# Optimization experiments

Measured on AMD Instinct MI355X. Metric: run time of the kernel, lower is better.

The kernel has to match this reference:

```python
import jax, jax.numpy as jnp
import numpy as np

N_Q, N_T, D, C = 4096, 8192, 512, 16
SIGMA = 2.0


def setup_inputs() -> dict:
    key = jax.random.key(0)
    k1, k2, k3 = jax.random.split(key, 3)
    X = jax.random.normal(k1, (N_Q, D), dtype=jnp.float32)
    X_train = jax.random.normal(k2, (N_T, D), dtype=jnp.float32)
    y = jax.random.randint(k3, (N_T,), 0, C, dtype=jnp.int32)
    sigma = jnp.float32(SIGMA)
    return {"X": X, "X_train": X_train, "y": y, "sigma": sigma}


def reference(X, X_train, y, sigma):
    xx = jnp.sum(X * X, axis=1, keepdims=True)              # [N_q, 1]
    tt = jnp.sum(X_train * X_train, axis=1)                 # [N_t]
    cross = jnp.einsum('qd,td->qt', X, X_train)             # [N_q, N_t]
    dist2 = jnp.maximum(xx + tt[None, :] - 2.0 * cross, 0.0)
    pattern = jnp.exp(-dist2 / (2.0 * sigma ** 2))          # Gaussian RBF kernel [N_q, N_t]
    # per-class segment sum over training patterns (replaces per-class Python loop)
    summation = jax.ops.segment_sum(pattern.T, y, num_segments=C).T  # [N_q, C]
    summation = summation / jnp.sum(summation, axis=1, keepdims=True)
    return jnp.argmax(summation, axis=1)
```

## Files before the change

### kernel.cpp

```cpp
#include <hip/hip_runtime.h>


#define NQ 4096
#define NT 8192
#define DD 512
#define NC 16
#define LN_FLT_MIN -87.336544750402f
#define SCREEN_T 730.0f

typedef __attribute__((ext_vector_type(4))) int   v4i;
typedef __attribute__((ext_vector_type(8))) int   v8i;
typedef __attribute__((ext_vector_type(16))) float f32x16;

__global__ __launch_bounds__(256) void prep_k(const float* __restrict__ X,
                                              const float* __restrict__ XT,
                                              unsigned char* __restrict__ fXp,
                                              unsigned char* __restrict__ fTp,
                                              float* __restrict__ xx,
                                              float* __restrict__ tt,
                                              float* __restrict__ classacc) {
  const int lane = threadIdx.x & 63;
  const int row  = blockIdx.x * 4 + (threadIdx.x >> 6);
  const float* src; unsigned char* dst; float* nrm; int r;
  if (row < NT) { r = row; src = XT + (size_t)r * DD; dst = fTp; nrm = tt + r; }
  else { r = row - NT; src = X + (size_t)r * DD; dst = fXp; nrm = xx + r; }
  const float4* s4 = (const float4*)src;
  const float4 a = s4[lane * 2], b = s4[lane * 2 + 1];
  int w0 = __builtin_amdgcn_cvt_pk_fp8_f32(a.x, a.y, 0, false);
  w0     = __builtin_amdgcn_cvt_pk_fp8_f32(a.z, a.w, w0, true);
  int w1 = __builtin_amdgcn_cvt_pk_fp8_f32(b.x, b.y, 0, false);
  w1     = __builtin_amdgcn_cvt_pk_fp8_f32(b.z, b.w, w1, true);
  int2 o; o.x = w0; o.y = w1;
  const int l = (r & 31) + 32 * ((lane >> 2) & 1);
  const size_t dest = ((size_t)(r >> 5) * 8 + (lane >> 3)) * 2048
                    + ((lane >> 1) & 1) * 1024 + l * 16 + (lane & 1) * 8;
  *(int2*)(dst + dest) = o;
  float acc = a.x*a.x + a.y*a.y + a.z*a.z + a.w*a.w
            + b.x*b.x + b.y*b.y + b.z*b.z + b.w*b.w;
  #pragma unroll
  for (int off = 32; off; off >>= 1) acc += __shfl_down(acc, off, 64);
  if (lane == 0) *nrm = acc;
  if (blockIdx.x < 64) {
    float4 z = {0.f, 0.f, 0.f, 0.f};
    ((float4*)classacc)[blockIdx.x * 256 + threadIdx.x] = z;
  }
}

#define MFMA(A, B, C) __builtin_amdgcn_mfma_scale_f32_32x32x64_f8f6f4( \
    (A), (B), (C), 0, 0, 0, 127, 0, 127)
#define BAR() __builtin_amdgcn_s_barrier()
#define WAITV(N) asm volatile("s_waitcnt vmcnt(" #N ")" ::: "memory")

static __device__ __forceinline__ void gll(const unsigned char* src, char* dst) {
  __builtin_amdgcn_global_load_lds(
      (const __attribute__((address_space(1))) unsigned int*)src,
      (__attribute__((address_space(3))) unsigned int*)dst, 16, 0, 0);
}

static __device__ __forceinline__ v8i ld32(const char* p) {
  v4i lo = *(const v4i*)p;
  v4i hi = *(const v4i*)(p + 1024);
  return __builtin_shufflevector(lo, hi, 0, 1, 2, 3, 4, 5, 6, 7);
}

__global__ __launch_bounds__(512) void pnn_mfma(const unsigned char* __restrict__ fXp,
                                                const unsigned char* __restrict__ fTp,
                                                const float* __restrict__ Xf,
                                                const float* __restrict__ Tf,
                                                const int* __restrict__ y,
                                                const float* __restrict__ sigp,
                                                const float* __restrict__ xx,
                                                const float* __restrict__ tt,
                                                float* __restrict__ classacc) {
  __shared__ char lds[49152];
  const int tid  = threadIdx.x;
  const int wid  = tid >> 6, lane = tid & 63;
  const int la   = lane & 31, lb = lane >> 5;
  const int wr   = wid >> 2, wc = wid & 3;

  const int bid = blockIdx.x;
  const int xcd = bid & 7, cc = bid >> 3;
  const int qt  = (xcd & 3) * 8 + (cc >> 4);
  const int tn  = (xcd >> 2) * 16 + (cc & 15);
  const int qbase = qt * 128, tbase = tn * 256;
  const int qrt0 = qbase >> 5;
  const int trt0 = tbase >> 5;

  const int sc = tid >> 7;
  const int si = (tid & 127) * 16;

#define STAGE(kt, Ab, Bb) { \
    gll(fXp + ((size_t)(qrt0 + sc) * 8 + (kt)) * 2048 + si, (Ab) + sc * 2048 + si); \
    gll(fTp + ((size_t)(trt0 + sc) * 8 + (kt)) * 2048 + si, (Bb) + sc * 2048 + si); \
    gll(fTp + ((size_t)(trt0 + sc + 4) * 8 + (kt)) * 2048 + si, (Bb) + (sc + 4) * 2048 + si); }

  char* const A0 = lds;
  char* const A1 = lds + 8192;
  char* const B0 = lds + 16384;
  char* const B1 = lds + 32768;

  f32x16 acc00 = (f32x16)(0.f), acc01 = (f32x16)(0.f);
  f32x16 acc10 = (f32x16)(0.f), acc11 = (f32x16)(0.f);

  STAGE(0, A0, B0)

  #pragma unroll
  for (int kt = 0; kt < 8; ++kt) {
    char* const Ac = (kt & 1) ? A1 : A0;
    char* const Bc = (kt & 1) ? B1 : B0;
    char* const An = (kt & 1) ? A0 : A1;
    char* const Bn = (kt & 1) ? B0 : B1;
    if (kt < 7) { STAGE(kt + 1, An, Bn) }
    if (kt < 7) { WAITV(3); } else { WAITV(0); }
    BAR();
    const v8i a0 = ld32(Ac + (wr * 2 + 0) * 2048 + lane * 16);
    const v8i a1 = ld32(Ac + (wr * 2 + 1) * 2048 + lane * 16);
    const v8i b0 = ld32(Bc + (wc * 2 + 0) * 2048 + lane * 16);
    const v8i b1 = ld32(Bc + (wc * 2 + 1) * 2048 + lane * 16);
    __builtin_amdgcn_s_setprio(1);
    acc00 = MFMA(a0, b0, acc00);
    acc01 = MFMA(a0, b1, acc01);
    acc10 = MFMA(a1, b0, acc10);
    acc11 = MFMA(a1, b1, acc11);
    __builtin_amdgcn_s_setprio(0);
    if (kt < 7) BAR();
  }
#undef STAGE

  const int wq = qbase + wr * 64;
  const int wt = tbase + wc * 64;
  const float sg = sigp[0];
  const float inv2s2 = 1.0f / (2.0f * sg * sg);
  float tnorm[2]; int tcls[2];
  #pragma unroll
  for (int nt = 0; nt < 2; ++nt) {
    const int t = wt + nt * 32 + la;
    tnorm[nt] = tt[t]; tcls[nt] = y[t];
  }

#define EPIL(ACC, mt, nt) { \
    _Pragma("unroll") \
    for (int reg = 0; reg < 16; ++reg) { \
      const int q = wq + (mt) * 32 + (reg & 3) + 8 * (reg >> 2) + 4 * lb; \
      const float xq = xx[q]; \
      const float d2 = xq + tnorm[(nt)] - 2.0f * (ACC)[reg]; \
      if (__builtin_expect(d2 < SCREEN_T, 0)) { \
        const int t = wt + (nt) * 32 + la; \
        const float4* xp = (const float4*)(Xf + (size_t)q * DD); \
        const float4* tp = (const float4*)(Tf + (size_t)t * DD); \
        float s0 = 0.f, s1 = 0.f, s2 = 0.f, s3 = 0.f; \
        for (int d = 0; d < DD / 4; ++d) { \
          const float4 xv = xp[d], tv = tp[d]; \
          s0 = fmaf(xv.x, tv.x, s0); s1 = fmaf(xv.y, tv.y, s1); \
          s2 = fmaf(xv.z, tv.z, s2); s3 = fmaf(xv.w, tv.w, s3); \
        } \
        const float dot = (s0 + s1) + (s2 + s3); \
        const float dd2 = fmaxf(xq + tnorm[(nt)] - 2.0f * dot, 0.f); \
        const float arg = -dd2 * inv2s2; \
        if (arg >= LN_FLT_MIN)             \
          atomicAdd(&classacc[q * NC + tcls[(nt)]], expf(arg)); \
      } \
    } }

  EPIL(acc00, 0, 0)
  EPIL(acc01, 0, 1)
  EPIL(acc10, 1, 0)
  EPIL(acc11, 1, 1)
#undef EPIL
}

__global__ __launch_bounds__(256) void argmax_k(const float* __restrict__ classacc,
                                                float* __restrict__ out) {
  const int q = blockIdx.x * 256 + threadIdx.x;
  float sc[NC];
  #pragma unroll
  for (int c4 = 0; c4 < 4; ++c4) {
    const float4 v = ((const float4*)(classacc + (size_t)q * NC))[c4];
    sc[c4*4+0] = v.x; sc[c4*4+1] = v.y; sc[c4*4+2] = v.z; sc[c4*4+3] = v.w;
  }
  float rowsum = 0.f;
  #pragma unroll
  for (int c = 0; c < NC; ++c) rowsum += sc[c];
  int best = 0; float bv = sc[0];
  #pragma unroll
  for (int c = 1; c < NC; ++c)
    if (sc[c] > bv) { bv = sc[c]; best = c; }
  out[q] = (rowsum > 0.f) ? (float)best : 0.0f;
}

extern "C" void kernel_launch(void* const* d_in, const int* in_sizes, int n_in,
                              void* d_out, int out_size, void* d_ws, size_t ws_size,
                              hipStream_t stream) {
  const float* X  = (const float*)d_in[0];
  const float* XT = (const float*)d_in[1];
  const int*   y  = (const int*)d_in[2];
  const float* sg = (const float*)d_in[3];
  float* out = (float*)d_out;

  char* wsp = (char*)d_ws;
  unsigned char* fXp = (unsigned char*)wsp;
  unsigned char* fTp = fXp + (size_t)NQ * DD;
  float* tt       = (float*)(wsp + 8u * 1024u * 1024u);
  float* xx       = tt + NT;
  float* classacc = xx + NQ;

  prep_k<<<(NQ + NT) / 4, 256, 0, stream>>>(X, XT, fXp, fTp, xx, tt, classacc);
  pnn_mfma<<<1024, 512, 0, stream>>>(fXp, fTp, X, XT, y, sg, xx, tt, classacc);
  argmax_k<<<NQ / 256, 256, 0, stream>>>(classacc, out);
}
```

Measured before the change: 48.03 us.

## Switch screening GEMM from FP8 to FP4 with triple-buffered LDS pipeline

Quantizes inputs to FP4 (e2m1) instead of FP8 in the prep kernel, halving packed operand bytes, and runs the scaled MFMA in FP4 mode. The main loop now processes two K-halves per stage with a three-buffer LDS ring in dynamic shared memory, which removes the trailing barrier. The screening threshold is raised to compensate for the coarser distance estimate, which risks more exact FP32 fallback recomputations in the epilogue.

```diff
diff --git a/kernel.cpp b/kernel.cpp
--- a/kernel.cpp
+++ b/kernel.cpp
@@ -6,11 +6,18 @@
 #define DD 512
 #define NC 16
 #define LN_FLT_MIN -87.336544750402f
-#define SCREEN_T 730.0f
+#define SCREEN_T 750.0f
 
 typedef __attribute__((ext_vector_type(4))) int   v4i;
 typedef __attribute__((ext_vector_type(8))) int   v8i;
 typedef __attribute__((ext_vector_type(16))) float f32x16;
+
+static __device__ __forceinline__ unsigned f2fp4(float x) {
+  const float a = __builtin_fabsf(x);
+  unsigned i = (unsigned)(a >= 0.25f) + (a >= 0.75f) + (a >= 1.25f)
+             + (a >= 1.75f) + (a >= 2.5f) + (a >= 3.5f) + (a >= 5.0f);
+  return i | (x < 0.0f ? 8u : 0u);
+}
 
 __global__ __launch_bounds__(256) void prep_k(const float* __restrict__ X,
                                               const float* __restrict__ XT,
@@ -26,15 +33,14 @@
   else { r = row - NT; src = X + (size_t)r * DD; dst = fXp; nrm = xx + r; }
   const float4* s4 = (const float4*)src;
   const float4 a = s4[lane * 2], b = s4[lane * 2 + 1];
-  int w0 = __builtin_amdgcn_cvt_pk_fp8_f32(a.x, a.y, 0, false);
-  w0     = __builtin_amdgcn_cvt_pk_fp8_f32(a.z, a.w, w0, true);
-  int w1 = __builtin_amdgcn_cvt_pk_fp8_f32(b.x, b.y, 0, false);
-  w1     = __builtin_amdgcn_cvt_pk_fp8_f32(b.z, b.w, w1, true);
-  int2 o; o.x = w0; o.y = w1;
+  const unsigned word =  f2fp4(a.x)        | (f2fp4(a.y) << 4)
+                      | (f2fp4(a.z) << 8)  | (f2fp4(a.w) << 12)
+                      | (f2fp4(b.x) << 16) | (f2fp4(b.y) << 20)
+                      | (f2fp4(b.z) << 24) | (f2fp4(b.w) << 28);
   const int l = (r & 31) + 32 * ((lane >> 2) & 1);
-  const size_t dest = ((size_t)(r >> 5) * 8 + (lane >> 3)) * 2048
-                    + ((lane >> 1) & 1) * 1024 + l * 16 + (lane & 1) * 8;
-  *(int2*)(dst + dest) = o;
+  const size_t dest = ((size_t)(r >> 5) * 8 + (lane >> 3)) * 1024
+                    + l * 16 + (lane & 3) * 4;
+  *(unsigned*)(dst + dest) = word;
   float acc = a.x*a.x + a.y*a.y + a.z*a.z + a.w*a.w
             + b.x*b.x + b.y*b.y + b.z*b.z + b.w*b.w;
   #pragma unroll
@@ -46,8 +52,8 @@
   }
 }
 
-#define MFMA(A, B, C) __builtin_amdgcn_mfma_scale_f32_32x32x64_f8f6f4( \
-    (A), (B), (C), 0, 0, 0, 127, 0, 127)
+#define MFMA4(A, B, C) __builtin_amdgcn_mfma_scale_f32_32x32x64_f8f6f4( \
+    (A), (B), (C), 4, 4, 0, 127, 0, 127)
 #define BAR() __builtin_amdgcn_s_barrier()
 #define WAITV(N) asm volatile("s_waitcnt vmcnt(" #N ")" ::: "memory")
 
@@ -57,10 +63,9 @@
       (__attribute__((address_space(3))) unsigned int*)dst, 16, 0, 0);
 }
 
-static __device__ __forceinline__ v8i ld32(const char* p) {
-  v4i lo = *(const v4i*)p;
-  v4i hi = *(const v4i*)(p + 1024);
-  return __builtin_shufflevector(lo, hi, 0, 1, 2, 3, 4, 5, 6, 7);
+static __device__ __forceinline__ v8i ld16(const char* p) {
+  const v4i lo = *(const v4i*)p;
+  return __builtin_shufflevector(lo, lo, 0, 1, 2, 3, -1, -1, -1, -1);
 }
 
 __global__ __launch_bounds__(512) void pnn_mfma(const unsigned char* __restrict__ fXp,
@@ -72,58 +77,62 @@
                                                 const float* __restrict__ xx,
                                                 const float* __restrict__ tt,
                                                 float* __restrict__ classacc) {
-  __shared__ char lds[49152];
+  extern __shared__ char lds[];
   const int tid  = threadIdx.x;
-  const int wid  = tid >> 6, lane = tid & 63;
+  const int w    = tid >> 6, lane = tid & 63;
   const int la   = lane & 31, lb = lane >> 5;
-  const int wr   = wid >> 2, wc = wid & 3;
+  const int wr   = w >> 2, wc = w & 3;
 
   const int bid = blockIdx.x;
   const int xcd = bid & 7, cc = bid >> 3;
   const int qt  = (xcd & 3) * 8 + (cc >> 4);
   const int tn  = (xcd >> 2) * 16 + (cc & 15);
   const int qbase = qt * 128, tbase = tn * 256;
-  const int qrt0 = qbase >> 5;
-  const int trt0 = tbase >> 5;
-
-  const int sc = tid >> 7;
-  const int si = (tid & 127) * 16;
-
-#define STAGE(kt, Ab, Bb) { \
-    gll(fXp + ((size_t)(qrt0 + sc) * 8 + (kt)) * 2048 + si, (Ab) + sc * 2048 + si); \
-    gll(fTp + ((size_t)(trt0 + sc) * 8 + (kt)) * 2048 + si, (Bb) + sc * 2048 + si); \
-    gll(fTp + ((size_t)(trt0 + sc + 4) * 8 + (kt)) * 2048 + si, (Bb) + (sc + 4) * 2048 + si); }
-
-  char* const A0 = lds;
-  char* const A1 = lds + 8192;
-  char* const B0 = lds + 16384;
-  char* const B1 = lds + 32768;
+  const int qrt0 = qbase >> 5, trt0 = tbase >> 5;
+
+  const unsigned char* sb0 = fXp + ((size_t)(qrt0 + (w >> 1)) * 8 + (w & 1)) * 1024 + lane * 16;
+  const unsigned char* sb1 = fTp + ((size_t)(trt0 + (w >> 1)) * 8 + (w & 1)) * 1024 + lane * 16;
+  const unsigned char* sb2 = fTp + ((size_t)(trt0 + 4 + (w >> 1)) * 8 + (w & 1)) * 1024 + lane * 16;
+  const int d0 = w * 1024 + lane * 16;
+  const int d1 = (w + 8) * 1024 + lane * 16;
+  const int d2 = (w + 16) * 1024 + lane * 16;
+
+#define STAGE(s, bofs) { \
+    gll(sb0 + (size_t)(s) * 2048, lds + (bofs) + d0); \
+    gll(sb1 + (size_t)(s) * 2048, lds + (bofs) + d1); \
+    gll(sb2 + (size_t)(s) * 2048, lds + (bofs) + d2); }
 
   f32x16 acc00 = (f32x16)(0.f), acc01 = (f32x16)(0.f);
   f32x16 acc10 = (f32x16)(0.f), acc11 = (f32x16)(0.f);
 
-  STAGE(0, A0, B0)
-
-  #pragma unroll
-  for (int kt = 0; kt < 8; ++kt) {
-    char* const Ac = (kt & 1) ? A1 : A0;
-    char* const Bc = (kt & 1) ? B1 : B0;
-    char* const An = (kt & 1) ? A0 : A1;
-    char* const Bn = (kt & 1) ? B0 : B1;
-    if (kt < 7) { STAGE(kt + 1, An, Bn) }
-    if (kt < 7) { WAITV(3); } else { WAITV(0); }
+  STAGE(0, 0)
+
+  #pragma unroll
+  for (int s = 0; s < 4; ++s) {
+    const int cur = (s % 3) * 24576;
+    const int nxt = ((s + 1) % 3) * 24576;
+    if (s < 3) { STAGE(s + 1, nxt) }
+    if (s < 3) { WAITV(3); } else { WAITV(0); }
     BAR();
-    const v8i a0 = ld32(Ac + (wr * 2 + 0) * 2048 + lane * 16);
-    const v8i a1 = ld32(Ac + (wr * 2 + 1) * 2048 + lane * 16);
-    const v8i b0 = ld32(Bc + (wc * 2 + 0) * 2048 + lane * 16);
-    const v8i b1 = ld32(Bc + (wc * 2 + 1) * 2048 + lane * 16);
+    const char* Bp = lds + cur;
+    const v8i a00 = ld16(Bp + ((wr * 2 + 0) * 2 + 0) * 1024 + lane * 16);
+    const v8i a10 = ld16(Bp + ((wr * 2 + 1) * 2 + 0) * 1024 + lane * 16);
+    const v8i b00 = ld16(Bp + (8 + (wc * 2 + 0) * 2 + 0) * 1024 + lane * 16);
+    const v8i b10 = ld16(Bp + (8 + (wc * 2 + 1) * 2 + 0) * 1024 + lane * 16);
+    const v8i a01 = ld16(Bp + ((wr * 2 + 0) * 2 + 1) * 1024 + lane * 16);
+    const v8i a11 = ld16(Bp + ((wr * 2 + 1) * 2 + 1) * 1024 + lane * 16);
+    const v8i b01 = ld16(Bp + (8 + (wc * 2 + 0) * 2 + 1) * 1024 + lane * 16);
+    const v8i b11 = ld16(Bp + (8 + (wc * 2 + 1) * 2 + 1) * 1024 + lane * 16);
     __builtin_amdgcn_s_setprio(1);
-    acc00 = MFMA(a0, b0, acc00);
-    acc01 = MFMA(a0, b1, acc01);
-    acc10 = MFMA(a1, b0, acc10);
-    acc11 = MFMA(a1, b1, acc11);
+    acc00 = MFMA4(a00, b00, acc00);
+    acc01 = MFMA4(a00, b10, acc01);
+    acc10 = MFMA4(a10, b00, acc10);
+    acc11 = MFMA4(a10, b10, acc11);
+    acc00 = MFMA4(a01, b01, acc00);
+    acc01 = MFMA4(a01, b11, acc01);
+    acc10 = MFMA4(a11, b01, acc10);
+    acc11 = MFMA4(a11, b11, acc11);
     __builtin_amdgcn_s_setprio(0);
-    if (kt < 7) BAR();
   }
 #undef STAGE
 
@@ -199,12 +208,15 @@
 
   char* wsp = (char*)d_ws;
   unsigned char* fXp = (unsigned char*)wsp;
-  unsigned char* fTp = fXp + (size_t)NQ * DD;
-  float* tt       = (float*)(wsp + 8u * 1024u * 1024u);
+  unsigned char* fTp = fXp + (size_t)NQ * DD / 2;
+  float* tt       = (float*)(wsp + 4u * 1024u * 1024u);
   float* xx       = tt + NT;
   float* classacc = xx + NQ;
 
+  (void)hipFuncSetAttribute((const void*)pnn_mfma,
+                            hipFuncAttributeMaxDynamicSharedMemorySize, 73728);
+
   prep_k<<<(NQ + NT) / 4, 256, 0, stream>>>(X, XT, fXp, fTp, xx, tt, classacc);
-  pnn_mfma<<<1024, 512, 0, stream>>>(fXp, fTp, X, XT, y, sg, xx, tt, classacc);
+  pnn_mfma<<<1024, 512, 73728, stream>>>(fXp, fTp, X, XT, y, sg, xx, tt, classacc);
   argmax_k<<<NQ / 256, 256, 0, stream>>>(classacc, out);
 }
```

Result: slower. 50.98 us (+6.1%).
